# Kernel tuning notes

Measured on AMD Instinct MI355X. Metric: run time of the kernel, lower is better.

The kernel has to match this reference:

```python
import jax, jax.numpy as jnp
import numpy as np

N, E, F, H = 50000, 800000, 64, 4
NEG_SLOPE = 0.2
LN_EPS = 1e-5


def setup_inputs() -> dict:
    key = jax.random.key(0)
    ks = jax.random.split(key, 12)
    h = jax.random.normal(ks[0], (N, F), dtype=jnp.float32)
    src = jax.random.randint(ks[1], (E,), 0, N, dtype=jnp.int32)
    dst = jax.random.randint(ks[2], (E,), 0, N, dtype=jnp.int32)
    s = 1.0 / np.sqrt(F)
    fc_w = jax.random.uniform(ks[3], (F, H * F), jnp.float32, -s, s)
    attn_l = jax.random.normal(ks[4], (H, F), dtype=jnp.float32) * s
    attn_r = jax.random.normal(ks[5], (H, F), dtype=jnp.float32) * s
    gat_bias = jnp.zeros((H * F,), dtype=jnp.float32)
    so = 1.0 / np.sqrt(H * F)
    out_w = jax.random.uniform(ks[6], (H * F, F), jnp.float32, -so, so)
    out_b = jax.random.uniform(ks[7], (F,), jnp.float32, -so, so)
    ln_g = jnp.ones((F,), dtype=jnp.float32)
    ln_b = jnp.zeros((F,), dtype=jnp.float32)
    return {"h": h, "src": src, "dst": dst, "fc_w": fc_w, "attn_l": attn_l,
            "attn_r": attn_r, "gat_bias": gat_bias, "out_w": out_w,
            "out_b": out_b, "ln_g": ln_g, "ln_b": ln_b}


def reference(h, src, dst, fc_w, attn_l, attn_r, gat_bias, out_w, out_b, ln_g, ln_b):
    # --- GATConv (DGL semantics) ---
    feat = (h @ fc_w).reshape(N, H, F)                      # [N,H,F]
    el = jnp.einsum('nhf,hf->nh', feat, attn_l)             # [N,H]
    er = jnp.einsum('nhf,hf->nh', feat, attn_r)             # [N,H]
    e = jax.nn.leaky_relu(el[src] + er[dst], NEG_SLOPE)     # [E,H]
    # edge softmax over incoming edges of each dst node
    m = jax.ops.segment_max(e, dst, num_segments=N)         # [N,H]
    ex = jnp.exp(e - m[dst])                                # [E,H]
    z = jax.ops.segment_sum(ex, dst, num_segments=N)        # [N,H]
    alpha = ex / z[dst]                                     # [E,H]
    msg = feat[src] * alpha[:, :, None]                     # [E,H,F]
    rst = jax.ops.segment_sum(msg, dst, num_segments=N)     # [N,H,F]
    rst = rst + gat_bias.reshape(H, F)
    # --- out linear + layernorm ---
    x = rst.reshape(N, H * F) @ out_w + out_b               # [N,F]
    mu = jnp.mean(x, axis=-1, keepdims=True)
    var = jnp.var(x, axis=-1, keepdims=True)
    return (x - mu) * jax.lax.rsqrt(var + LN_EPS) * ln_g + ln_b
```

## Files before the change

### kernel.cpp

```cpp
#include <hip/hip_runtime.h>

#define NN 50000
#define EE 800000
#define FF 64
#define HH 4
#define HF 256
#define NEG_SLOPE 0.2f
#define LN_EPS 1e-5f
#define WPACK_N (4 * 8 * 64 * 8)
#define NTILE (NN / 16)
#define TROW 264
#define NXCD 8
#define RCAP 32

typedef __attribute__((ext_vector_type(8))) short s8v;
typedef __attribute__((ext_vector_type(4))) float f4v;

__device__ __forceinline__ unsigned short f32_to_bf16_rne(float x) {
  unsigned int u = __float_as_uint(x);
  unsigned int r = u + 0x7FFFu + ((u >> 16) & 1u);
  return (unsigned short)(r >> 16);
}

__global__ __launch_bounds__(256) void k_prep(
    const float* __restrict__ fc_w, const float* __restrict__ out_w,
    const float* __restrict__ attn_l, const float* __restrict__ attn_r,
    const float* __restrict__ gat_bias, const float* __restrict__ out_b,
    unsigned short* __restrict__ wpack, float* __restrict__ alv,
    float* __restrict__ arv, float* __restrict__ outb2,
    int* __restrict__ cnt8) {
  const int idx = blockIdx.x * 256 + threadIdx.x;
  if (idx < WPACK_N) {
    const int j = idx & 7;
    const int l = (idx >> 3) & 63;
    const int t = (idx >> 9) & 7;
    const int ct = idx >> 12;
    const int k = 32 * t + (l >> 4) * 8 + j;
    const int c = 16 * ct + (l & 15);
    const int hh = k >> 6, kk = k & 63;
    const float* fw = fc_w + kk * HF + hh * FF;
    const float* ow = out_w + (size_t)(hh * FF) * FF + c;
    float acc = 0.f;
#pragma unroll
    for (int ff = 0; ff < FF; ++ff) acc = fmaf(fw[ff], ow[(size_t)ff * FF], acc);
    wpack[idx] = f32_to_bf16_rne(acc);
  } else if (idx < WPACK_N + 512) {
    const int i = idx - WPACK_N;
    const int hh = (i >> 6) & 3, kk = i & 63;
    const float* fw = fc_w + kk * HF + hh * FF;
    const float* at = (i < 256 ? attn_l : attn_r) + hh * FF;
    float acc = 0.f;
#pragma unroll
    for (int ff = 0; ff < FF; ++ff) acc = fmaf(fw[ff], at[ff], acc);
    (i < 256 ? alv : arv)[(hh << 6) | kk] = acc;
  } else if (idx < WPACK_N + 512 + FF) {
    const int c = idx - WPACK_N - 512;
    float acc = out_b[c];
    for (int k = 0; k < HF; ++k) acc = fmaf(gat_bias[k], out_w[(size_t)k * FF + c], acc);
    outb2[c] = acc;
  }
  if (idx < NXCD * NN) cnt8[idx] = 0;
}

__global__ __launch_bounds__(256) void k_elr(
    const float* __restrict__ h, const float* __restrict__ alv,
    const float* __restrict__ arv, unsigned short* __restrict__ hb,
    float* __restrict__ el, float* __restrict__ er) {
  const int wave = threadIdx.x >> 6;
  const int lane = threadIdx.x & 63;
  const int row = blockIdx.x * 32 + wave * 8 + (lane >> 3);
  if (row >= NN) return;
  const int kc = (lane & 7) * 8;

  float hv[8];
  *(float4*)hv = *(const float4*)(h + (size_t)row * FF + kc);
  *(float4*)(hv + 4) = *(const float4*)(h + (size_t)row * FF + kc + 4);

  unsigned pk[4];
#pragma unroll
  for (int jj = 0; jj < 4; ++jj)
    pk[jj] = (unsigned)f32_to_bf16_rne(hv[2 * jj]) |
             ((unsigned)f32_to_bf16_rne(hv[2 * jj + 1]) << 16);
  *(uint4*)(hb + (size_t)row * FF + kc) = make_uint4(pk[0], pk[1], pk[2], pk[3]);

  float p[8];
#pragma unroll
  for (int hh = 0; hh < 4; ++hh) {
    const float* av = alv + (hh << 6) + kc;
    const float* bv = arv + (hh << 6) + kc;
    float sa = 0.f, sb = 0.f;
#pragma unroll
    for (int j = 0; j < 8; ++j) {
      sa = fmaf(hv[j], av[j], sa);
      sb = fmaf(hv[j], bv[j], sb);
    }
    p[hh] = sa; p[4 + hh] = sb;
  }
#pragma unroll
  for (int off = 1; off < 8; off <<= 1) {
#pragma unroll
    for (int q = 0; q < 8; ++q) p[q] += __shfl_xor(p[q], off, 64);
  }
  const int q = lane & 7;
  if (q < 4) el[(size_t)row * 4 + q] = p[q];
  else       er[(size_t)row * 4 + (q - 4)] = p[q];
}

__global__ __launch_bounds__(256) void k_scatter(
    const int* __restrict__ src, const int* __restrict__ dst,
    int* __restrict__ cnt8, unsigned short* __restrict__ colp8) {
  unsigned xcd;
  asm("s_getreg_b32 %0, hwreg(HW_REG_XCC_ID)" : "=s"(xcd));
  xcd &= 7;
  int* cb = cnt8 + xcd * NN;
  unsigned short* pb = colp8 + (size_t)xcd * NN * RCAP;
  const int e4 = (blockIdx.x * 256 + threadIdx.x) * 4;
  if (e4 + 3 < EE) {
    const int4 d4 = *(const int4*)(dst + e4);
    const int4 s4 = *(const int4*)(src + e4);
    const int p0 = __hip_atomic_fetch_add(&cb[d4.x], 1, __ATOMIC_RELAXED,
                                          __HIP_MEMORY_SCOPE_WORKGROUP);
    const int p1 = __hip_atomic_fetch_add(&cb[d4.y], 1, __ATOMIC_RELAXED,
                                          __HIP_MEMORY_SCOPE_WORKGROUP);
    const int p2 = __hip_atomic_fetch_add(&cb[d4.z], 1, __ATOMIC_RELAXED,
                                          __HIP_MEMORY_SCOPE_WORKGROUP);
    const int p3 = __hip_atomic_fetch_add(&cb[d4.w], 1, __ATOMIC_RELAXED,
                                          __HIP_MEMORY_SCOPE_WORKGROUP);
    if (p0 < RCAP) pb[d4.x * RCAP + p0] = (unsigned short)s4.x;
    if (p1 < RCAP) pb[d4.y * RCAP + p1] = (unsigned short)s4.y;
    if (p2 < RCAP) pb[d4.z * RCAP + p2] = (unsigned short)s4.z;
    if (p3 < RCAP) pb[d4.w * RCAP + p3] = (unsigned short)s4.w;
  } else {
    for (int j = 0; j < 4; ++j) {
      const int e = e4 + j;
      if (e < EE) {
        const int d = dst[e];
        const int sv = src[e];
        const int pos = __hip_atomic_fetch_add(&cb[d], 1, __ATOMIC_RELAXED,
                                               __HIP_MEMORY_SCOPE_WORKGROUP);
        if (pos < RCAP) pb[d * RCAP + pos] = (unsigned short)sv;
      }
    }
  }
}

__global__ __launch_bounds__(256) void k_gather_out(
    const unsigned short* __restrict__ hb, const float* __restrict__ el,
    const float* __restrict__ er, const int* __restrict__ cnt8,
    const unsigned short* __restrict__ colp8,
    const unsigned short* __restrict__ wpack, const float* __restrict__ outb2,
    const float* __restrict__ ln_g, const float* __restrict__ ln_b,
    float* __restrict__ out) {
  __shared__ unsigned short tile[16][TROW];
  __shared__ float part[4][16][2];
  __shared__ unsigned short xa[4][2560];
  const int wave = threadIdx.x >> 6;
  const int lane = threadIdx.x & 63;
  const int n0 = blockIdx.x * 16;
  const int nbase = n0 + wave * 4;
  unsigned short* Xw = &xa[wave][0];
  unsigned short* Aw = &xa[wave][2048];

  int cgrp = 0;
  if (lane < 32) cgrp = cnt8[(lane >> 2) * NN + nbase + (lane & 3)];
  cgrp = cgrp > RCAP ? RCAP : cgrp;
  int inc = cgrp;
#pragma unroll
  for (int off = 4; off <= 16; off <<= 1) {
    const int t = __shfl_up(inc, off, 64);
    if (lane >= off) inc += t;
  }
  const int exc = inc - cgrp;

#pragma unroll
  for (int r = 0; r < 4; ++r) {
    const int row = wave * 4 + r;
    const int n = nbase + r;
    const float4 erv = *(const float4*)(er + (size_t)n * 4);

    const int mi = __builtin_amdgcn_readlane(inc, 28 + r);
    const int m = mi > 64 ? 64 : mi;
    const int p1 = __builtin_amdgcn_readlane(exc, 4 + r);
    const int p2 = __builtin_amdgcn_readlane(exc, 8 + r);
    const int p3 = __builtin_amdgcn_readlane(exc, 12 + r);
    const int p4 = __builtin_amdgcn_readlane(exc, 16 + r);
    const int p5 = __builtin_amdgcn_readlane(exc, 20 + r);
    const int p6 = __builtin_amdgcn_readlane(exc, 24 + r);
    const int p7 = __builtin_amdgcn_readlane(exc, 28 + r);
    int seg = 0, pb = 0;
    if (lane >= p1) { seg = 1; pb = p1; }
    if (lane >= p2) { seg = 2; pb = p2; }
    if (lane >= p3) { seg = 3; pb = p3; }
    if (lane >= p4) { seg = 4; pb = p4; }
    if (lane >= p5) { seg = 5; pb = p5; }
    if (lane >= p6) { seg = 6; pb = p6; }
    if (lane >= p7) { seg = 7; pb = p7; }
    int s = 0;
    if (lane < m)
      s = colp8[((size_t)seg * NN + n) * RCAP + (lane - pb)];

    float w0 = 0.f, w1 = 0.f, w2 = 0.f, w3 = 0.f;
    if (lane < m) {
      const float4 elv = *(const float4*)(el + (size_t)s * 4);
      float e0 = elv.x + erv.x, e1 = elv.y + erv.y;
      float e2 = elv.z + erv.z, e3 = elv.w + erv.w;
      e0 = e0 > 0.f ? e0 : NEG_SLOPE * e0;
      e1 = e1 > 0.f ? e1 : NEG_SLOPE * e1;
      e2 = e2 > 0.f ? e2 : NEG_SLOPE * e2;
      e3 = e3 > 0.f ? e3 : NEG_SLOPE * e3;
      w0 = __expf(e0); w1 = __expf(e1);
      w2 = __expf(e2); w3 = __expf(e3);
    }
    float z0 = w0, z1 = w1, z2 = w2, z3 = w3;
#pragma unroll
    for (int off = 1; off < 64; off <<= 1) {
      z0 += __shfl_xor(z0, off, 64);
      z1 += __shfl_xor(z1, off, 64);
      z2 += __shfl_xor(z2, off, 64);
      z3 += __shfl_xor(z3, off, 64);
    }
    w0 *= (z0 > 0.f ? 1.f / z0 : 0.f);
    w1 *= (z1 > 0.f ? 1.f / z1 : 0.f);
    w2 *= (z2 > 0.f ? 1.f / z2 : 0.f);
    w3 *= (z3 > 0.f ? 1.f / z3 : 0.f);

    if (lane < 32) {
      const int ai = ((lane >> 3) << 7) | (lane & 7);
      Aw[ai]      = f32_to_bf16_rne(w0);
      Aw[ai + 32] = f32_to_bf16_rne(w1);
      Aw[ai + 64] = f32_to_bf16_rne(w2);
      Aw[ai + 96] = f32_to_bf16_rne(w3);
    }

#pragma unroll
    for (int e = 0; e < 32; e += 8) {
      unsigned short t0, t1, t2, t3, t4, t5, t6, t7;
      t0 = hb[((unsigned)__builtin_amdgcn_readlane(s, e + 0) << 6) + lane];
      t1 = hb[((unsigned)__builtin_amdgcn_readlane(s, e + 1) << 6) + lane];
      t2 = hb[((unsigned)__builtin_amdgcn_readlane(s, e + 2) << 6) + lane];
      t3 = hb[((unsigned)__builtin_amdgcn_readlane(s, e + 3) << 6) + lane];
      t4 = hb[((unsigned)__builtin_amdgcn_readlane(s, e + 4) << 6) + lane];
      t5 = hb[((unsigned)__builtin_amdgcn_readlane(s, e + 5) << 6) + lane];
      t6 = hb[((unsigned)__builtin_amdgcn_readlane(s, e + 6) << 6) + lane];
      t7 = hb[((unsigned)__builtin_amdgcn_readlane(s, e + 7) << 6) + lane];
      const unsigned u0 = (unsigned)t0 | ((unsigned)t1 << 16);
      const unsigned u1 = (unsigned)t2 | ((unsigned)t3 << 16);
      const unsigned u2 = (unsigned)t4 | ((unsigned)t5 << 16);
      const unsigned u3 = (unsigned)t6 | ((unsigned)t7 << 16);
      const int gsw = (lane & 7) ^ (lane >> 3) ^ (e >> 3);
      *(uint4*)(Xw + ((e + (lane >> 3)) << 6) + (gsw << 3)) =
          make_uint4(u0, u1, u2, u3);
    }

    const s8v af = *(const s8v*)(Aw + (((lane >> 4) << 7) | ((lane & 15) << 3)));
    f4v acc[4];
#pragma unroll
    for (int ct = 0; ct < 4; ++ct) {
      const f4v z4 = {0.f, 0.f, 0.f, 0.f};
      const int f = lane & 15;
      const int rowr = ((lane >> 4) << 3) + (ct << 1) + (f >> 3);
      const int gsr = (f & 7) ^ ((ct << 1) + (f >> 3)) ^ (lane >> 4);
      const s8v bf = *(const s8v*)(Xw + (rowr << 6) + (gsr << 3));
      acc[ct] = __builtin_amdgcn_mfma_f32_16x16x32_bf16(af, bf, z4, 0, 0, 0);
    }

    if (m > 32) {
      if (lane >= 32) {
        const int e2 = lane - 32;
        const int ai = ((e2 >> 3) << 7) | (e2 & 7);
        Aw[ai]      = f32_to_bf16_rne(w0);
        Aw[ai + 32] = f32_to_bf16_rne(w1);
        Aw[ai + 64] = f32_to_bf16_rne(w2);
        Aw[ai + 96] = f32_to_bf16_rne(w3);
      }
#pragma unroll
      for (int e = 32; e < 64; e += 8) {
        unsigned short t0, t1, t2, t3, t4, t5, t6, t7;
        t0 = hb[((unsigned)__builtin_amdgcn_readlane(s, e + 0) << 6) + lane];
        t1 = hb[((unsigned)__builtin_amdgcn_readlane(s, e + 1) << 6) + lane];
        t2 = hb[((unsigned)__builtin_amdgcn_readlane(s, e + 2) << 6) + lane];
        t3 = hb[((unsigned)__builtin_amdgcn_readlane(s, e + 3) << 6) + lane];
        t4 = hb[((unsigned)__builtin_amdgcn_readlane(s, e + 4) << 6) + lane];
        t5 = hb[((unsigned)__builtin_amdgcn_readlane(s, e + 5) << 6) + lane];
        t6 = hb[((unsigned)__builtin_amdgcn_readlane(s, e + 6) << 6) + lane];
        t7 = hb[((unsigned)__builtin_amdgcn_readlane(s, e + 7) << 6) + lane];
        const unsigned u0 = (unsigned)t0 | ((unsigned)t1 << 16);
        const unsigned u1 = (unsigned)t2 | ((unsigned)t3 << 16);
        const unsigned u2 = (unsigned)t4 | ((unsigned)t5 << 16);
        const unsigned u3 = (unsigned)t6 | ((unsigned)t7 << 16);
        const int eb = e - 32;
        const int gsw = (lane & 7) ^ (lane >> 3) ^ (eb >> 3);
        *(uint4*)(Xw + ((eb + (lane >> 3)) << 6) + (gsw << 3)) =
            make_uint4(u0, u1, u2, u3);
      }
      const s8v af2 = *(const s8v*)(Aw + (((lane >> 4) << 7) | ((lane & 15) << 3)));
#pragma unroll
      for (int ct = 0; ct < 4; ++ct) {
        const int f = lane & 15;
        const int rowr = ((lane >> 4) << 3) + (ct << 1) + (f >> 3);
        const int gsr = (f & 7) ^ ((ct << 1) + (f >> 3)) ^ (lane >> 4);
        const s8v bf = *(const s8v*)(Xw + (rowr << 6) + (gsr << 3));
        acc[ct] = __builtin_amdgcn_mfma_f32_16x16x32_bf16(af2, bf, acc[ct], 0, 0, 0);
      }
    }

    const int q = lane >> 4, r2 = lane & 15;
#pragma unroll
    for (int ct = 0; ct < 4; ++ct)
      tile[row][(q << 6) | (ct << 4) | r2] = f32_to_bf16_rne(acc[ct][0]);
  }
  __syncthreads();

  const int cl = lane & 15;
  const int quad = lane >> 4;
  s8v a[8];
#pragma unroll
  for (int t = 0; t < 8; ++t)
    a[t] = *(const s8v*)(&tile[cl][32 * t + quad * 8]);

  f4v acc = {0.f, 0.f, 0.f, 0.f};
#pragma unroll
  for (int t = 0; t < 8; ++t) {
    const s8v b = *(const s8v*)(wpack + ((wave * 8 + t) * 64 + lane) * 8);
    acc = __builtin_amdgcn_mfma_f32_16x16x32_bf16(a[t], b, acc, 0, 0, 0);
  }

  const float ob = outb2[16 * wave + cl];
  float xv[4];
#pragma unroll
  for (int r = 0; r < 4; ++r) {
    const float v = acc[r] + ob;
    xv[r] = v;
    float p1 = v, p2 = v * v;
#pragma unroll
    for (int off = 1; off < 16; off <<= 1) {
      p1 += __shfl_xor(p1, off, 64);
      p2 += __shfl_xor(p2, off, 64);
    }
    if (cl == 0) {
      part[wave][quad * 4 + r][0] = p1;
      part[wave][quad * 4 + r][1] = p2;
    }
  }
  __syncthreads();
#pragma unroll
  for (int r = 0; r < 4; ++r) {
    const int row = quad * 4 + r;
    const float t1 = part[0][row][0] + part[1][row][0] +
                     part[2][row][0] + part[3][row][0];
    const float t2 = part[0][row][1] + part[1][row][1] +
                     part[2][row][1] + part[3][row][1];
    const float mu = t1 * (1.f / 64.f);
    const float var = t2 * (1.f / 64.f) - mu * mu;
    const float inv = rsqrtf(var + LN_EPS);
    const int c = 16 * wave + cl;
    out[(size_t)(n0 + row) * FF + c] = (xv[r] - mu) * inv * ln_g[c] + ln_b[c];
  }
}

extern "C" void kernel_launch(void* const* d_in, const int* in_sizes, int n_in,
                              void* d_out, int out_size, void* d_ws,
                              size_t ws_size, hipStream_t stream) {
  const float* h_in   = (const float*)d_in[0];
  const int*   src    = (const int*)d_in[1];
  const int*   dst    = (const int*)d_in[2];
  const float* fc_w   = (const float*)d_in[3];
  const float* attn_l = (const float*)d_in[4];
  const float* attn_r = (const float*)d_in[5];
  const float* gbias  = (const float*)d_in[6];
  const float* out_w  = (const float*)d_in[7];
  const float* out_b  = (const float*)d_in[8];
  const float* ln_g   = (const float*)d_in[9];
  const float* ln_b   = (const float*)d_in[10];
  float* out = (float*)d_out;

  char* p = (char*)d_ws;
  auto alloc = [&](size_t bytes) {
    char* q = p;
    p += (bytes + 255) & ~(size_t)255;
    return q;
  };
  unsigned short* hb     = (unsigned short*)alloc((size_t)NN * FF * 2);
  unsigned short* wpack  = (unsigned short*)alloc((size_t)WPACK_N * 2);
  float* alv     = (float*)alloc(256 * 4);
  float* arv     = (float*)alloc(256 * 4);
  float* outb2   = (float*)alloc(64 * 4);
  float* el      = (float*)alloc((size_t)NN * HH * 4);
  float* er      = (float*)alloc((size_t)NN * HH * 4);
  int*   cnt8    = (int*)alloc((size_t)NXCD * NN * 4);
  unsigned short* colp8 =
      (unsigned short*)alloc((size_t)NXCD * NN * RCAP * 2);

  k_prep<<<(NXCD * NN + 255) / 256, 256, 0, stream>>>(
      fc_w, out_w, attn_l, attn_r, gbias, out_b, wpack, alv, arv, outb2, cnt8);
  k_elr<<<(NN + 31) / 32, 256, 0, stream>>>(h_in, alv, arv, hb, el, er);
  k_scatter<<<(EE / 4 + 255) / 256, 256, 0, stream>>>(src, dst, cnt8, colp8);
  k_gather_out<<<NTILE, 256, 0, stream>>>(hb, el, er, cnt8, colp8, wpack,
                                          outb2, ln_g, ln_b, out);
}
```

Before: 189.6 us.

## Merge scatter, weight packing and el/er projection into one heterogeneous launch

The counter zeroing moves to hipMemsetAsync and the tiny attention/bias projections move to a 3-block kernel. The CSR-bucket scatter, the fused weight packing and the per-node el/er/bf16 conversion then run as disjoint block ranges of a single launch. This removes two kernel boundaries and lets the atomic-heavy scatter overlap with the compute-bound packing and projection work. The cost is an extra memset and a small kernel on the stream, plus possible load imbalance between block roles.

```diff
diff --git a/kernel.cpp b/kernel.cpp
--- a/kernel.cpp
+++ b/kernel.cpp
@@ -12,6 +12,9 @@
 #define TROW 264
 #define NXCD 8
 #define RCAP 32
+#define SCATB ((EE / 4 + 255) / 256)
+#define WPB (WPACK_N / 256)
+#define ELRB ((NN + 31) / 32)
 
 typedef __attribute__((ext_vector_type(8))) short s8v;
 typedef __attribute__((ext_vector_type(4))) float f4v;
@@ -22,15 +25,77 @@
   return (unsigned short)(r >> 16);
 }
 
-__global__ __launch_bounds__(256) void k_prep(
+__global__ __launch_bounds__(256) void k_small(
+    const float* __restrict__ fc_w, const float* __restrict__ attn_l,
+    const float* __restrict__ attn_r, const float* __restrict__ gat_bias,
+    const float* __restrict__ out_w, const float* __restrict__ out_b,
+    float* __restrict__ alv, float* __restrict__ arv,
+    float* __restrict__ outb2) {
+  const int gid = blockIdx.x * 256 + threadIdx.x;
+  if (gid < 512) {
+    const int hh = (gid >> 6) & 3, kk = gid & 63;
+    const float* fw = fc_w + kk * HF + hh * FF;
+    const float* at = (gid < 256 ? attn_l : attn_r) + hh * FF;
+    float acc = 0.f;
+#pragma unroll
+    for (int ff = 0; ff < FF; ++ff) acc = fmaf(fw[ff], at[ff], acc);
+    (gid < 256 ? alv : arv)[(hh << 6) | kk] = acc;
+  } else if (gid < 512 + FF) {
+    const int c = gid - 512;
+    float acc = out_b[c];
+    for (int k = 0; k < HF; ++k)
+      acc = fmaf(gat_bias[k], out_w[(size_t)k * FF + c], acc);
+    outb2[c] = acc;
+  }
+}
+
+__global__ __launch_bounds__(256) void k_fused(
+    const int* __restrict__ src, const int* __restrict__ dst,
+    int* __restrict__ cnt8, unsigned short* __restrict__ colp8,
     const float* __restrict__ fc_w, const float* __restrict__ out_w,
-    const float* __restrict__ attn_l, const float* __restrict__ attn_r,
-    const float* __restrict__ gat_bias, const float* __restrict__ out_b,
-    unsigned short* __restrict__ wpack, float* __restrict__ alv,
-    float* __restrict__ arv, float* __restrict__ outb2,
-    int* __restrict__ cnt8) {
-  const int idx = blockIdx.x * 256 + threadIdx.x;
-  if (idx < WPACK_N) {
+    unsigned short* __restrict__ wpack, const float* __restrict__ h,
+    const float* __restrict__ alv, const float* __restrict__ arv,
+    unsigned short* __restrict__ hb, float* __restrict__ el,
+    float* __restrict__ er) {
+  const int bid = blockIdx.x;
+  if (bid < SCATB) {
+    unsigned xcd;
+    asm("s_getreg_b32 %0, hwreg(HW_REG_XCC_ID)" : "=s"(xcd));
+    xcd &= 7;
+    int* cb = cnt8 + xcd * NN;
+    unsigned short* pb = colp8 + (size_t)xcd * NN * RCAP;
+    const int e4 = (bid * 256 + threadIdx.x) * 4;
+    if (e4 + 3 < EE) {
+      const int4 d4 = *(const int4*)(dst + e4);
+      const int4 s4 = *(const int4*)(src + e4);
+      const int p0 = __hip_atomic_fetch_add(&cb[d4.x], 1, __ATOMIC_RELAXED,
+                                            __HIP_MEMORY_SCOPE_WORKGROUP);
+      const int p1 = __hip_atomic_fetch_add(&cb[d4.y], 1, __ATOMIC_RELAXED,
+                                            __HIP_MEMORY_SCOPE_WORKGROUP);
+      const int p2 = __hip_atomic_fetch_add(&cb[d4.z], 1, __ATOMIC_RELAXED,
+                                            __HIP_MEMORY_SCOPE_WORKGROUP);
+      const int p3 = __hip_atomic_fetch_add(&cb[d4.w], 1, __ATOMIC_RELAXED,
+                                            __HIP_MEMORY_SCOPE_WORKGROUP);
+      if (p0 < RCAP) pb[d4.x * RCAP + p0] = (unsigned short)s4.x;
+      if (p1 < RCAP) pb[d4.y * RCAP + p1] = (unsigned short)s4.y;
+      if (p2 < RCAP) pb[d4.z * RCAP + p2] = (unsigned short)s4.z;
+      if (p3 < RCAP) pb[d4.w * RCAP + p3] = (unsigned short)s4.w;
+    } else {
+      for (int j = 0; j < 4; ++j) {
+        const int e = e4 + j;
+        if (e < EE) {
+          const int d = dst[e];
+          const int sv = src[e];
+          const int pos = __hip_atomic_fetch_add(&cb[d], 1, __ATOMIC_RELAXED,
+                                                 __HIP_MEMORY_SCOPE_WORKGROUP);
+          if (pos < RCAP) pb[d * RCAP + pos] = (unsigned short)sv;
+        }
+      }
+    }
+    return;
+  }
+  if (bid < SCATB + WPB) {
+    const int idx = (bid - SCATB) * 256 + threadIdx.x;
     const int j = idx & 7;
     const int l = (idx >> 3) & 63;
     const int t = (idx >> 9) & 7;
@@ -44,31 +109,11 @@
 #pragma unroll
     for (int ff = 0; ff < FF; ++ff) acc = fmaf(fw[ff], ow[(size_t)ff * FF], acc);
     wpack[idx] = f32_to_bf16_rne(acc);
-  } else if (idx < WPACK_N + 512) {
-    const int i = idx - WPACK_N;
-    const int hh = (i >> 6) & 3, kk = i & 63;
-    const float* fw = fc_w + kk * HF + hh * FF;
-    const float* at = (i < 256 ? attn_l : attn_r) + hh * FF;
-    float acc = 0.f;
-#pragma unroll
-    for (int ff = 0; ff < FF; ++ff) acc = fmaf(fw[ff], at[ff], acc);
-    (i < 256 ? alv : arv)[(hh << 6) | kk] = acc;
-  } else if (idx < WPACK_N + 512 + FF) {
-    const int c = idx - WPACK_N - 512;
-    float acc = out_b[c];
-    for (int k = 0; k < HF; ++k) acc = fmaf(gat_bias[k], out_w[(size_t)k * FF + c], acc);
-    outb2[c] = acc;
-  }
-  if (idx < NXCD * NN) cnt8[idx] = 0;
-}
-
-__global__ __launch_bounds__(256) void k_elr(
-    const float* __restrict__ h, const float* __restrict__ alv,
-    const float* __restrict__ arv, unsigned short* __restrict__ hb,
-    float* __restrict__ el, float* __restrict__ er) {
+    return;
+  }
   const int wave = threadIdx.x >> 6;
   const int lane = threadIdx.x & 63;
-  const int row = blockIdx.x * 32 + wave * 8 + (lane >> 3);
+  const int row = (bid - SCATB - WPB) * 32 + wave * 8 + (lane >> 3);
   if (row >= NN) return;
   const int kc = (lane & 7) * 8;
 
@@ -104,44 +149,6 @@
   const int q = lane & 7;
   if (q < 4) el[(size_t)row * 4 + q] = p[q];
   else       er[(size_t)row * 4 + (q - 4)] = p[q];
-}
-
-__global__ __launch_bounds__(256) void k_scatter(
-    const int* __restrict__ src, const int* __restrict__ dst,
-    int* __restrict__ cnt8, unsigned short* __restrict__ colp8) {
-  unsigned xcd;
-  asm("s_getreg_b32 %0, hwreg(HW_REG_XCC_ID)" : "=s"(xcd));
-  xcd &= 7;
-  int* cb = cnt8 + xcd * NN;
-  unsigned short* pb = colp8 + (size_t)xcd * NN * RCAP;
-  const int e4 = (blockIdx.x * 256 + threadIdx.x) * 4;
-  if (e4 + 3 < EE) {
-    const int4 d4 = *(const int4*)(dst + e4);
-    const int4 s4 = *(const int4*)(src + e4);
-    const int p0 = __hip_atomic_fetch_add(&cb[d4.x], 1, __ATOMIC_RELAXED,
-                                          __HIP_MEMORY_SCOPE_WORKGROUP);
-    const int p1 = __hip_atomic_fetch_add(&cb[d4.y], 1, __ATOMIC_RELAXED,
-                                          __HIP_MEMORY_SCOPE_WORKGROUP);
-    const int p2 = __hip_atomic_fetch_add(&cb[d4.z], 1, __ATOMIC_RELAXED,
-                                          __HIP_MEMORY_SCOPE_WORKGROUP);
-    const int p3 = __hip_atomic_fetch_add(&cb[d4.w], 1, __ATOMIC_RELAXED,
-                                          __HIP_MEMORY_SCOPE_WORKGROUP);
-    if (p0 < RCAP) pb[d4.x * RCAP + p0] = (unsigned short)s4.x;
-    if (p1 < RCAP) pb[d4.y * RCAP + p1] = (unsigned short)s4.y;
-    if (p2 < RCAP) pb[d4.z * RCAP + p2] = (unsigned short)s4.z;
-    if (p3 < RCAP) pb[d4.w * RCAP + p3] = (unsigned short)s4.w;
-  } else {
-    for (int j = 0; j < 4; ++j) {
-      const int e = e4 + j;
-      if (e < EE) {
-        const int d = dst[e];
-        const int sv = src[e];
-        const int pos = __hip_atomic_fetch_add(&cb[d], 1, __ATOMIC_RELAXED,
-                                               __HIP_MEMORY_SCOPE_WORKGROUP);
-        if (pos < RCAP) pb[d * RCAP + pos] = (unsigned short)sv;
-      }
-    }
-  }
 }
 
 __global__ __launch_bounds__(256) void k_gather_out(
@@ -391,10 +398,11 @@
   unsigned short* colp8 =
       (unsigned short*)alloc((size_t)NXCD * NN * RCAP * 2);
 
-  k_prep<<<(NXCD * NN + 255) / 256, 256, 0, stream>>>(
-      fc_w, out_w, attn_l, attn_r, gbias, out_b, wpack, alv, arv, outb2, cnt8);
-  k_elr<<<(NN + 31) / 32, 256, 0, stream>>>(h_in, alv, arv, hb, el, er);
-  k_scatter<<<(EE / 4 + 255) / 256, 256, 0, stream>>>(src, dst, cnt8, colp8);
+  hipMemsetAsync(cnt8, 0, (size_t)NXCD * NN * 4, stream);
+  k_small<<<3, 256, 0, stream>>>(fc_w, attn_l, attn_r, gbias, out_w, out_b,
+                                 alv, arv, outb2);
+  k_fused<<<SCATB + WPB + ELRB, 256, 0, stream>>>(
+      src, dst, cnt8, colp8, fc_w, out_w, wpack, h_in, alv, arv, hb, el, er);
   k_gather_out<<<NTILE, 256, 0, stream>>>(hb, el, er, cnt8, colp8, wpack,
                                           outb2, ln_g, ln_b, out);
 }
```

Measured after the change: 194.3 us. +2.5%, slower.
